# Performance work log

Measured on AMD Instinct MI355X. Metric: run time of the kernel, lower is better.

Reference implementation:

```python
import math
import jax, jax.numpy as jnp
import numpy as np

B, T, DIN, DH, E, TOPK = 2048, 512, 32, 96, 6, 2


def setup_inputs() -> dict:
    key = jax.random.key(0)
    ks = jax.random.split(key, 20)
    x = jax.random.normal(ks[0], (B, T, DIN), jnp.float32)
    lengths = jax.random.randint(ks[1], (B,), 1, T + 1)
    mask = (jnp.arange(T)[None, :] < lengths[:, None])

    def U(k, shape, fan):
        s = 1.0 / math.sqrt(fan)
        return jax.random.uniform(k, shape, jnp.float32, -s, s)

    # PyTorch LSTM init: U(-1/sqrt(DH), 1/sqrt(DH)); gate order i,f,g,o
    Wih = U(ks[2], (4 * DH, DIN), DH)
    Whh = U(ks[3], (4 * DH, DH), DH)
    bih = U(ks[4], (4 * DH,), DH)
    bhh = U(ks[5], (4 * DH,), DH)
    Wq = U(ks[6], (DH, DH), DH); bq = U(ks[7], (DH,), DH)
    Wk = U(ks[8], (DH, DH), DH); bk = U(ks[9], (DH,), DH)
    Wv = U(ks[10], (DH, DH), DH); bv = U(ks[11], (DH,), DH)
    Wg = U(ks[12], (E, 2 * DH), 2 * DH); bg = U(ks[13], (E,), 2 * DH)
    We1 = U(ks[14], (E, DH, 2 * DH), 2 * DH); be1 = U(ks[15], (E, DH), 2 * DH)
    We2 = U(ks[16], (E, DH), DH); be2 = U(ks[17], (E,), DH)
    return dict(x=x, lengths=lengths, mask=mask, Wih=Wih, Whh=Whh, bih=bih, bhh=bhh,
                Wq=Wq, bq=bq, Wk=Wk, bk=bk, Wv=Wv, bv=bv, Wg=Wg, bg=bg,
                We1=We1, be1=be1, We2=We2, be2=be2)


def _lstm(x, mask, Wih, Whh, bih, bhh):
    # packed-sequence semantics: carry frozen past each sample's length,
    # padded output positions zeroed (like pad_packed_sequence).
    xg = x @ Wih.T + bih  # [B,T,4*DH] precomputed input projection
    dh = Whh.shape[1]

    def step(carry, inp):
        h, c = carry
        xg_t, m_t = inp
        g = xg_t + h @ Whh.T + bhh
        i, f, gg, o = jnp.split(g, 4, axis=-1)
        c_new = jax.nn.sigmoid(f) * c + jax.nn.sigmoid(i) * jnp.tanh(gg)
        h_new = jax.nn.sigmoid(o) * jnp.tanh(c_new)
        m = m_t[:, None]
        h = jnp.where(m, h_new, h)
        c = jnp.where(m, c_new, c)
        return (h, c), jnp.where(m, h_new, 0.0)

    init = (jnp.zeros((x.shape[0], dh), x.dtype), jnp.zeros((x.shape[0], dh), x.dtype))
    (hT, _), H = jax.lax.scan(step, init, (jnp.swapaxes(xg, 0, 1), mask.T))
    return jnp.swapaxes(H, 0, 1), hT  # H:[B,T,DH], hT:[B,DH]


def reference(x, lengths, mask, Wih, Whh, bih, bhh, Wq, bq, Wk, bk, Wv, bv,
              Wg, bg, We1, be1, We2, be2):
    H, hT = _lstm(x, mask, Wih, Whh, bih, bhh)
    Q = hT @ Wq.T + bq                      # [B,DH]
    K = H @ Wk.T + bk                       # [B,T,DH]
    V = H @ Wv.T + bv                       # [B,T,DH]
    logits = jnp.einsum('bd,btd->bt', Q, K) / math.sqrt(K.shape[-1])
    logits = jnp.where(mask, logits, -1e9)
    alpha = jax.nn.softmax(logits, axis=1)  # [B,T]
    ctx = jnp.einsum('bt,btd->bd', alpha, V)
    feats = jnp.concatenate([ctx, hT], axis=-1)  # [B,2*DH]
    gate_logits = feats @ Wg.T + bg              # [B,E]
    topv, topi = jax.lax.top_k(gate_logits, TOPK)
    pi = jax.nn.softmax(topv, axis=-1)           # [B,TOPK]
    # all-expert dense compute (E tiny), then gather selected -> same math as
    # the per-expert masked scatter loop in the torch module (dropout off).
    h1 = jax.nn.relu(jnp.einsum('bf,ehf->beh', feats, We1) + be1[None])  # [B,E,DH]
    outs = jnp.einsum('beh,eh->be', h1, We2) + be2[None]                  # [B,E]
    sel = jnp.take_along_axis(outs, topi, axis=1)                         # [B,TOPK]
    yhat = jnp.sum(pi * sel, axis=-1, keepdims=True)                      # [B,1]
    return yhat, alpha, gate_logits
```

## Files before the change

kernel.cpp:

```cpp
#include <hip/hip_runtime.h>
#include <hip/hip_bf16.h>

#define B_ 2048
#define T_ 512
#define DIN_ 32
#define DH_ 96
#define NG_ 384
#define E_ 6

#define BPB 8
#define HP 104
#define GS 10

typedef __attribute__((ext_vector_type(8))) _Float16 f16x8;
typedef __attribute__((ext_vector_type(4))) float f32x4;

#if defined(__has_builtin)
# if __has_builtin(__builtin_amdgcn_exp2f)
#  define EXP2F(x) __builtin_amdgcn_exp2f(x)
# endif
# if __has_builtin(__builtin_amdgcn_rcpf)
#  define RCPF(x) __builtin_amdgcn_rcpf(x)
# endif
#endif
#ifndef EXP2F
# define EXP2F(x) exp2f(x)
#endif
#ifndef RCPF
# define RCPF(x) (1.0f/(x))
#endif

__device__ __forceinline__ float sigf(float x) {
    return RCPF(1.0f + EXP2F(x * -1.44269504f));
}
__device__ __forceinline__ float tanhf_(float x) {
    return 1.0f - 2.0f * RCPF(1.0f + EXP2F(x * 2.88539008f));
}

__device__ __forceinline__ f16x8 cvt8(float4 a, float4 b) {
    f16x8 r;
    r[0] = (_Float16)a.x; r[1] = (_Float16)a.y; r[2] = (_Float16)a.z; r[3] = (_Float16)a.w;
    r[4] = (_Float16)b.x; r[5] = (_Float16)b.y; r[6] = (_Float16)b.z; r[7] = (_Float16)b.w;
    return r;
}
__device__ __forceinline__ f16x8 cvt8p(const float* p) {
    return cvt8(*(const float4*)p, *(const float4*)(p + 4));
}

__device__ __forceinline__ void lds_barrier() {
    asm volatile("s_waitcnt lgkmcnt(0)\n\ts_barrier" ::: "memory");
}

__global__ __launch_bounds__(512) void sort_kernel(
    const int* __restrict__ lengths, int* __restrict__ perm) {
    __shared__ int sbins[512];
    __shared__ int soffs[512];
    const int tid = threadIdx.x;
    sbins[tid] = 0;
    __syncthreads();
    for (int b = tid; b < B_; b += 512) atomicAdd(&sbins[lengths[b] - 1], 1);
    __syncthreads();
    soffs[tid] = sbins[tid];
    __syncthreads();
    for (int d = 1; d < 512; d <<= 1) {
        int v = (tid >= d) ? soffs[tid - d] : 0;
        __syncthreads();
        soffs[tid] += v;
        __syncthreads();
    }
    int excl = soffs[tid] - sbins[tid];
    __syncthreads();
    soffs[tid] = excl;
    __syncthreads();
    for (int b = tid; b < B_; b += 512) {
        const int pos = atomicAdd(&soffs[lengths[b] - 1], 1);
        perm[pos] = b;
    }
}

__global__ __launch_bounds__(768, 1) void lstm_kernel(
    const float* __restrict__ x, const int* __restrict__ lengths,
    const int* __restrict__ perm,
    const float* __restrict__ Wih, const float* __restrict__ Whh,
    const float* __restrict__ bih, const float* __restrict__ bhh,
    _Float16* __restrict__ Hout, float* __restrict__ hT)
{
    __shared__ float sgate[NG_ * GS];
    __shared__ _Float16 sh[2][16 * HP];
    __shared__ int sgb[BPB], slen[BPB];

    const int tid  = threadIdx.x;
    const int bb   = blockIdx.x * BPB;
    const int wave = tid >> 6;
    const int lane = tid & 63;
    const int col  = lane & 15;
    const int quad = lane >> 4;

    if (tid < BPB) {
        const int g = perm[bb + tid];
        sgb[tid] = g;
        slen[tid] = lengths[g];
    }
    {
        _Float16* shf = &sh[0][0];
        for (int i = tid; i < 2 * 16 * HP; i += 768) shf[i] = (_Float16)0.f;
    }
    __syncthreads();

    int bmax = slen[0];
#pragma unroll
    for (int i = 1; i < BPB; ++i) bmax = max(bmax, slen[i]);

    int gc[2]; float bias[2];
    f16x8 wh[2][3], wi[2];
#pragma unroll
    for (int j = 0; j < 2; ++j) {
        const int tau = wave * 2 + j;
        const int g = tau / 6, u6 = tau % 6;
        const int gcj = g * DH_ + u6 * 16 + col;
        gc[j] = gcj;
#pragma unroll
        for (int kf = 0; kf < 3; ++kf)
            wh[j][kf] = cvt8p(Whh + gcj * DH_ + kf * 32 + quad * 8);
        wi[j] = cvt8p(Wih + gcj * DIN_ + quad * 8);
        bias[j] = bih[gcj] + bhh[gcj];
    }

    const int eu = tid >> 3;
    const int eb = tid & 7;
    float c1 = 0.f, hk1 = 0.f;
    const int len1 = slen[eb];

    const bool st_act = tid < 384;
    const int sb = tid / 48;
    const int su = (tid % 48) * 2;
    _Float16* Hst = Hout + ((long long)sgb[sb] * T_) * DH_ + su;

    const float* xp = x + ((long long)sgb[col & 7] * T_) * DIN_ + quad * 8;
    float4 xc0 = *(const float4*)xp;
    float4 xc1 = *(const float4*)(xp + 4);

    for (int t = 0; t < bmax; ++t) {
        const int buf = t & 1;

        const _Float16* hrow = &sh[buf][col * HP];
        f16x8 h0 = *(const f16x8*)(hrow + 0  + quad * 8);
        f16x8 h1 = *(const f16x8*)(hrow + 32 + quad * 8);
        f16x8 h2 = *(const f16x8*)(hrow + 64 + quad * 8);

        const float* xpn = (t + 1 < T_) ? (xp + DIN_) : xp;
        float4 xn0 = *(const float4*)xpn;
        float4 xn1 = *(const float4*)(xpn + 4);

        f16x8 xa = cvt8(xc0, xc1);

#pragma unroll
        for (int j = 0; j < 2; ++j) {
            f32x4 a = {bias[j], bias[j], bias[j], bias[j]};
            a = __builtin_amdgcn_mfma_f32_16x16x32_f16(h0, wh[j][0], a, 0, 0, 0);
            a = __builtin_amdgcn_mfma_f32_16x16x32_f16(h1, wh[j][1], a, 0, 0, 0);
            a = __builtin_amdgcn_mfma_f32_16x16x32_f16(h2, wh[j][2], a, 0, 0, 0);
            a = __builtin_amdgcn_mfma_f32_16x16x32_f16(xa, wi[j],    a, 0, 0, 0);
            if (quad < 2) {
                float2* sp = (float2*)&sgate[gc[j] * GS + quad * 4];
                sp[0] = float2{a[0], a[1]};
                sp[1] = float2{a[2], a[3]};
            }
        }
        lds_barrier();

        if (t > 0 && st_act) {
            unsigned v = *(const unsigned*)&sh[buf][sb * HP + su];
            *(unsigned*)Hst = v;
            Hst += DH_;
        }

        {
            float iv = sgate[(0 * DH_ + eu) * GS + eb];
            float fv = sgate[(1 * DH_ + eu) * GS + eb];
            float gv = sgate[(2 * DH_ + eu) * GS + eb];
            float ov = sgate[(3 * DH_ + eu) * GS + eb];
            float cn = sigf(fv) * c1 + sigf(iv) * tanhf_(gv);
            float hn = sigf(ov) * tanhf_(cn);
            const bool m = t < len1;
            c1  = m ? cn : c1;
            hk1 = m ? hn : hk1;
            sh[buf ^ 1][eb * HP + eu] = (_Float16)hk1;
        }
        lds_barrier();

        xp = xpn; xc0 = xn0; xc1 = xn1;
    }

    if (st_act) {
        unsigned v = *(const unsigned*)&sh[bmax & 1][sb * HP + su];
        *(unsigned*)Hst = v;
    }

    hT[sgb[eb] * DH_ + eu] = hk1;
}

__global__ __launch_bounds__(512) void attn_moe_kernel(
    const _Float16* __restrict__ H, const float* __restrict__ hT,
    const int* __restrict__ lengths,
    const float* __restrict__ Wq, const float* __restrict__ bq,
    const float* __restrict__ Wk, const float* __restrict__ bk,
    const float* __restrict__ Wv, const float* __restrict__ bv,
    const float* __restrict__ Wg, const float* __restrict__ bg,
    const float* __restrict__ We1, const float* __restrict__ be1,
    const float* __restrict__ We2, const float* __restrict__ be2,
    float* __restrict__ yhat_out, float* __restrict__ alpha_out,
    float* __restrict__ gl_out)
{
    __shared__ float salpha[T_];
    __shared__ float shT[DH_];
    __shared__ float sQ[DH_];
    __shared__ float sqk[DH_];
    __shared__ float spart[4 * DH_];
    __shared__ float sfeats[2 * DH_];
    __shared__ float sh1[2][DH_];
    __shared__ float sred[8], ssum[8];
    __shared__ float sgl[E_];
    __shared__ float spi[2];
    __shared__ float souts[2];
    __shared__ float sqb_s;
    __shared__ int stopi[2];

    const int b = blockIdx.x, tid = threadIdx.x;
    const int len = lengths[b];
    const float scale = 0.10206207262f;

    if (tid < DH_) shT[tid] = hT[b * DH_ + tid];
    __syncthreads();
    if (tid < DH_) {
        float acc = bq[tid];
        const float* wr = Wq + tid * DH_;
        for (int d = 0; d < DH_; d += 4) {
            float4 w4 = *(const float4*)(wr + d);
            acc += w4.x * shT[d] + w4.y * shT[d + 1] + w4.z * shT[d + 2] + w4.w * shT[d + 3];
        }
        sQ[tid] = acc;
    }
    __syncthreads();
    if (tid < DH_) {
        float acc = 0.f;
        for (int j = 0; j < DH_; ++j) acc += Wk[j * DH_ + tid] * sQ[j];
        sqk[tid] = acc * scale;
    }
    if (tid >= 448) {
        const int ln = tid - 448;
        float p = sQ[ln] * bk[ln];
        if (ln < DH_ - 64) p += sQ[ln + 64] * bk[ln + 64];
        for (int off = 32; off; off >>= 1) p += __shfl_xor(p, off);
        if (ln == 0) sqb_s = p * scale;
    }
    __syncthreads();
    const float qbv = sqb_s;

    const bool valid = tid < len;
    float l = qbv;
    if (valid) {
        const _Float16* hr = H + ((long long)b * T_ + tid) * DH_;
#pragma unroll
        for (int u = 0; u < DH_; u += 8) {
            f16x8 hv = *(const f16x8*)(hr + u);
            float4 qa = *(const float4*)&sqk[u];
            float4 qc = *(const float4*)&sqk[u + 4];
            l += (float)hv[0] * qa.x + (float)hv[1] * qa.y
               + (float)hv[2] * qa.z + (float)hv[3] * qa.w
               + (float)hv[4] * qc.x + (float)hv[5] * qc.y
               + (float)hv[6] * qc.z + (float)hv[7] * qc.w;
        }
    }
    float lv = valid ? l : -1e30f;

    float m = lv;
    for (int off = 32; off; off >>= 1) m = fmaxf(m, __shfl_xor(m, off));
    if ((tid & 63) == 0) sred[tid >> 6] = m;
    __syncthreads();
    m = sred[0];
#pragma unroll
    for (int i = 1; i < 8; ++i) m = fmaxf(m, sred[i]);

    float e = valid ? EXP2F((l - m) * 1.44269504f) : 0.f;
    float s = e;
    for (int off = 32; off; off >>= 1) s += __shfl_xor(s, off);
    if ((tid & 63) == 0) ssum[tid >> 6] = s;
    __syncthreads();
    s = ssum[0];
#pragma unroll
    for (int i = 1; i < 8; ++i) s += ssum[i];

    const float alpha = e * RCPF(s);
    salpha[tid] = alpha;
    alpha_out[(long long)b * T_ + tid] = alpha;
    __syncthreads();

    if (tid < 4 * DH_) {
        const int s4 = tid / DH_, u = tid - s4 * DH_;
        float acc = 0.f;
        const int t0 = s4 * 128, t1 = min(t0 + 128, len);
        const _Float16* hc = H + ((long long)b * T_) * DH_ + u;
        for (int t = t0; t < t1; ++t)
            acc += salpha[t] * (float)hc[t * DH_];
        spart[s4 * DH_ + u] = acc;
    }
    __syncthreads();
    if (tid < DH_) {
        float craw = spart[tid] + spart[DH_ + tid] + spart[2 * DH_ + tid] + spart[3 * DH_ + tid];
        spart[tid] = craw;
    }
    __syncthreads();
    if (tid < DH_) {
        float acc = bv[tid];
        const float* wr = Wv + tid * DH_;
        for (int u = 0; u < DH_; u += 4) {
            float4 w4 = *(const float4*)(wr + u);
            acc += w4.x * spart[u] + w4.y * spart[u + 1] + w4.z * spart[u + 2] + w4.w * spart[u + 3];
        }
        sfeats[tid] = acc;
        sfeats[DH_ + tid] = shT[tid];
    }
    __syncthreads();

    if (tid < 192) {
        const int e6 = tid >> 5, cc = tid & 31;
        float p = 0.f;
        const float* wg = Wg + e6 * 2 * DH_;
#pragma unroll
        for (int j = 0; j < 6; ++j) p += wg[cc * 6 + j] * sfeats[cc * 6 + j];
        for (int off = 16; off; off >>= 1) p += __shfl_xor(p, off);
        if (cc == 0) {
            float g = p + bg[e6];
            sgl[e6] = g;
            gl_out[b * E_ + e6] = g;
        }
    }
    __syncthreads();

    if (tid == 0) {
        int i0 = 0; float v0 = sgl[0];
        for (int ee = 1; ee < E_; ++ee) if (sgl[ee] > v0) { v0 = sgl[ee]; i0 = ee; }
        int i1 = -1; float v1 = -1e30f;
        for (int ee = 0; ee < E_; ++ee) {
            if (ee == i0) continue;
            if (sgl[ee] > v1) { v1 = sgl[ee]; i1 = ee; }
        }
        float e1 = EXP2F((v1 - v0) * 1.44269504f);
        float inv = RCPF(1.f + e1);
        spi[0] = inv; spi[1] = e1 * inv;
        stopi[0] = i0; stopi[1] = i1;
    }
    __syncthreads();

    if (tid < 192) {
        const int e2 = tid / DH_, u = tid - e2 * DH_;
        const int ex = stopi[e2];
        float acc = be1[ex * DH_ + u];
        const float* w = We1 + ((long long)ex * DH_ + u) * (2 * DH_);
        for (int f = 0; f < 2 * DH_; f += 4) {
            float4 w4 = *(const float4*)(w + f);
            acc += w4.x * sfeats[f] + w4.y * sfeats[f + 1] + w4.z * sfeats[f + 2] + w4.w * sfeats[f + 3];
        }
        sh1[e2][u] = fmaxf(acc, 0.f);
    }
    __syncthreads();

    if (tid < 128) {
        const int e2 = tid >> 6, ln = tid & 63;
        const int ex = stopi[e2];
        const float* w2 = We2 + ex * DH_;
        float p = sh1[e2][ln] * w2[ln];
        if (ln < DH_ - 64) p += sh1[e2][ln + 64] * w2[ln + 64];
        for (int off = 32; off; off >>= 1) p += __shfl_xor(p, off);
        if (ln == 0) souts[e2] = p + be2[ex];
    }
    __syncthreads();
    if (tid == 0)
        yhat_out[b] = spi[0] * souts[0] + spi[1] * souts[1];
}

extern "C" void kernel_launch(void* const* d_in, const int* in_sizes, int n_in,
                              void* d_out, int out_size, void* d_ws, size_t ws_size,
                              hipStream_t stream) {
    const float* x   = (const float*)d_in[0];
    const int* lengths = (const int*)d_in[1];
    const float* Wih = (const float*)d_in[3];
    const float* Whh = (const float*)d_in[4];
    const float* bih = (const float*)d_in[5];
    const float* bhh = (const float*)d_in[6];
    const float* Wq  = (const float*)d_in[7];
    const float* bq  = (const float*)d_in[8];
    const float* Wk  = (const float*)d_in[9];
    const float* bk  = (const float*)d_in[10];
    const float* Wv  = (const float*)d_in[11];
    const float* bv  = (const float*)d_in[12];
    const float* Wg  = (const float*)d_in[13];
    const float* bg  = (const float*)d_in[14];
    const float* We1 = (const float*)d_in[15];
    const float* be1 = (const float*)d_in[16];
    const float* We2 = (const float*)d_in[17];
    const float* be2 = (const float*)d_in[18];

    float* yhat  = (float*)d_out;
    float* alpha = yhat + B_;
    float* gl    = alpha + (size_t)B_ * T_;

    char* ws = (char*)d_ws;
    _Float16* Hws = (_Float16*)ws;
    float* hTws = (float*)(ws + (size_t)B_ * T_ * DH_ * 2);
    float* qkws = hTws + (size_t)B_ * DH_;
    float* qbws = qkws + (size_t)B_ * DH_;
    int* bins   = (int*)(qbws + B_);
    int* offs   = bins + 512;
    int* perm   = offs + 512;

    sort_kernel<<<dim3(1), dim3(512), 0, stream>>>(lengths, perm);

    lstm_kernel<<<dim3(B_ / BPB), dim3(768), 0, stream>>>(
        x, lengths, perm, Wih, Whh, bih, bhh, Hws, hTws);
    attn_moe_kernel<<<dim3(B_), dim3(512), 0, stream>>>(
        Hws, hTws, lengths, Wq, bq, Wk, bk, Wv, bv, Wg, bg,
        We1, be1, We2, be2, yhat, alpha, gl);
}
```

Measured before the change: 781.2 us.

## Shrink LSTM hidden buffer and restructure attention kernel to 256 threads

The LSTM kernel now keeps only the 8 real batch rows in its shared hidden-state buffer. The unused MFMA rows 8-15 are zero-filled in registers instead of being read from LDS and global memory. The attention/MoE kernel drops to 256 threads, each handling two timesteps for the logits and softmax. The context reduction now uses vectorized 8-wide f16 loads with shuffle reductions in place of scalar strided loads across 384 threads. Unused workspace pointers are also removed. The aim is less LDS traffic and better memory coalescing, at the cost of fewer threads per block in attention.

Measured after the change: 697.9 us. -10.7%, faster.

```diff
diff --git a/kernel.cpp b/kernel.cpp
--- a/kernel.cpp
+++ b/kernel.cpp
@@ -86,7 +86,7 @@
     _Float16* __restrict__ Hout, float* __restrict__ hT)
 {
     __shared__ float sgate[NG_ * GS];
-    __shared__ _Float16 sh[2][16 * HP];
+    __shared__ _Float16 sh[2][8 * HP];
     __shared__ int sgb[BPB], slen[BPB];
 
     const int tid  = threadIdx.x;
@@ -103,7 +103,7 @@
     }
     {
         _Float16* shf = &sh[0][0];
-        for (int i = tid; i < 2 * 16 * HP; i += 768) shf[i] = (_Float16)0.f;
+        for (int i = tid; i < 2 * 8 * HP; i += 768) shf[i] = (_Float16)0.f;
     }
     __syncthreads();
 
@@ -136,21 +136,25 @@
     const int su = (tid % 48) * 2;
     _Float16* Hst = Hout + ((long long)sgb[sb] * T_) * DH_ + su;
 
+    const bool arow = col < 8;
     const float* xp = x + ((long long)sgb[col & 7] * T_) * DIN_ + quad * 8;
-    float4 xc0 = *(const float4*)xp;
-    float4 xc1 = *(const float4*)(xp + 4);
+    float4 xc0 = make_float4(0.f, 0.f, 0.f, 0.f), xc1 = xc0;
+    if (arow) { xc0 = *(const float4*)xp; xc1 = *(const float4*)(xp + 4); }
 
     for (int t = 0; t < bmax; ++t) {
         const int buf = t & 1;
 
-        const _Float16* hrow = &sh[buf][col * HP];
-        f16x8 h0 = *(const f16x8*)(hrow + 0  + quad * 8);
-        f16x8 h1 = *(const f16x8*)(hrow + 32 + quad * 8);
-        f16x8 h2 = *(const f16x8*)(hrow + 64 + quad * 8);
+        f16x8 h0 = 0, h1 = 0, h2 = 0;
+        if (arow) {
+            const _Float16* hrow = &sh[buf][col * HP];
+            h0 = *(const f16x8*)(hrow + 0  + quad * 8);
+            h1 = *(const f16x8*)(hrow + 32 + quad * 8);
+            h2 = *(const f16x8*)(hrow + 64 + quad * 8);
+        }
 
         const float* xpn = (t + 1 < T_) ? (xp + DIN_) : xp;
-        float4 xn0 = *(const float4*)xpn;
-        float4 xn1 = *(const float4*)(xpn + 4);
+        float4 xn0 = make_float4(0.f, 0.f, 0.f, 0.f), xn1 = xn0;
+        if (arow) { xn0 = *(const float4*)xpn; xn1 = *(const float4*)(xpn + 4); }
 
         f16x8 xa = cvt8(xc0, xc1);
 
@@ -200,7 +204,7 @@
     hT[sgb[eb] * DH_ + eu] = hk1;
 }
 
-__global__ __launch_bounds__(512) void attn_moe_kernel(
+__global__ __launch_bounds__(256) void attn_moe_kernel(
     const _Float16* __restrict__ H, const float* __restrict__ hT,
     const int* __restrict__ lengths,
     const float* __restrict__ Wq, const float* __restrict__ bq,
@@ -216,10 +220,10 @@
     __shared__ float shT[DH_];
     __shared__ float sQ[DH_];
     __shared__ float sqk[DH_];
-    __shared__ float spart[4 * DH_];
+    __shared__ float spart[DH_];
     __shared__ float sfeats[2 * DH_];
     __shared__ float sh1[2][DH_];
-    __shared__ float sred[8], ssum[8];
+    __shared__ float sred[4], ssum[4];
     __shared__ float sgl[E_];
     __shared__ float spi[2];
     __shared__ float souts[2];
@@ -247,8 +251,8 @@
         for (int j = 0; j < DH_; ++j) acc += Wk[j * DH_ + tid] * sQ[j];
         sqk[tid] = acc * scale;
     }
-    if (tid >= 448) {
-        const int ln = tid - 448;
+    if (tid >= 192) {
+        const int ln = tid - 192;
         float p = sQ[ln] * bk[ln];
         if (ln < DH_ - 64) p += sQ[ln + 64] * bk[ln + 64];
         for (int off = 32; off; off >>= 1) p += __shfl_xor(p, off);
@@ -257,60 +261,78 @@
     __syncthreads();
     const float qbv = sqb_s;
 
-    const bool valid = tid < len;
-    float l = qbv;
-    if (valid) {
-        const _Float16* hr = H + ((long long)b * T_ + tid) * DH_;
-#pragma unroll
-        for (int u = 0; u < DH_; u += 8) {
-            f16x8 hv = *(const f16x8*)(hr + u);
-            float4 qa = *(const float4*)&sqk[u];
-            float4 qc = *(const float4*)&sqk[u + 4];
-            l += (float)hv[0] * qa.x + (float)hv[1] * qa.y
-               + (float)hv[2] * qa.z + (float)hv[3] * qa.w
-               + (float)hv[4] * qc.x + (float)hv[5] * qc.y
-               + (float)hv[6] * qc.z + (float)hv[7] * qc.w;
-        }
-    }
-    float lv = valid ? l : -1e30f;
-
-    float m = lv;
+    float lg[2]; bool vd[2];
+#pragma unroll
+    for (int hh = 0; hh < 2; ++hh) {
+        const int t = tid + hh * 256;
+        vd[hh] = t < len;
+        float l = qbv;
+        if (vd[hh]) {
+            const _Float16* hr = H + ((long long)b * T_ + t) * DH_;
+#pragma unroll
+            for (int u = 0; u < DH_; u += 8) {
+                f16x8 hv = *(const f16x8*)(hr + u);
+                float4 qa = *(const float4*)&sqk[u];
+                float4 qc = *(const float4*)&sqk[u + 4];
+                l += (float)hv[0] * qa.x + (float)hv[1] * qa.y
+                   + (float)hv[2] * qa.z + (float)hv[3] * qa.w
+                   + (float)hv[4] * qc.x + (float)hv[5] * qc.y
+                   + (float)hv[6] * qc.z + (float)hv[7] * qc.w;
+            }
+        }
+        lg[hh] = l;
+    }
+
+    float m = fmaxf(vd[0] ? lg[0] : -1e30f, vd[1] ? lg[1] : -1e30f);
     for (int off = 32; off; off >>= 1) m = fmaxf(m, __shfl_xor(m, off));
     if ((tid & 63) == 0) sred[tid >> 6] = m;
     __syncthreads();
-    m = sred[0];
-#pragma unroll
-    for (int i = 1; i < 8; ++i) m = fmaxf(m, sred[i]);
-
-    float e = valid ? EXP2F((l - m) * 1.44269504f) : 0.f;
-    float s = e;
+    m = fmaxf(fmaxf(sred[0], sred[1]), fmaxf(sred[2], sred[3]));
+
+    float e0 = vd[0] ? EXP2F((lg[0] - m) * 1.44269504f) : 0.f;
+    float e1 = vd[1] ? EXP2F((lg[1] - m) * 1.44269504f) : 0.f;
+    float s = e0 + e1;
     for (int off = 32; off; off >>= 1) s += __shfl_xor(s, off);
     if ((tid & 63) == 0) ssum[tid >> 6] = s;
     __syncthreads();
-    s = ssum[0];
-#pragma unroll
-    for (int i = 1; i < 8; ++i) s += ssum[i];
-
-    const float alpha = e * RCPF(s);
-    salpha[tid] = alpha;
-    alpha_out[(long long)b * T_ + tid] = alpha;
-    __syncthreads();
-
-    if (tid < 4 * DH_) {
-        const int s4 = tid / DH_, u = tid - s4 * DH_;
-        float acc = 0.f;
-        const int t0 = s4 * 128, t1 = min(t0 + 128, len);
-        const _Float16* hc = H + ((long long)b * T_) * DH_ + u;
-        for (int t = t0; t < t1; ++t)
-            acc += salpha[t] * (float)hc[t * DH_];
-        spart[s4 * DH_ + u] = acc;
-    }
-    __syncthreads();
-    if (tid < DH_) {
-        float craw = spart[tid] + spart[DH_ + tid] + spart[2 * DH_ + tid] + spart[3 * DH_ + tid];
-        spart[tid] = craw;
-    }
-    __syncthreads();
+    s = (ssum[0] + ssum[1]) + (ssum[2] + ssum[3]);
+
+    const float rinv = RCPF(s);
+    const float a0 = e0 * rinv, a1 = e1 * rinv;
+    salpha[tid] = a0;
+    salpha[tid + 256] = a1;
+    alpha_out[(long long)b * T_ + tid] = a0;
+    alpha_out[(long long)b * T_ + tid + 256] = a1;
+    __syncthreads();
+
+    if (tid < 192) {
+        const int ub = tid >> 4, tl = tid & 15;
+        float acc[8] = {0.f, 0.f, 0.f, 0.f, 0.f, 0.f, 0.f, 0.f};
+        const _Float16* hb = H + ((long long)b * T_) * DH_ + ub * 8;
+#pragma unroll 4
+        for (int k = 0; k < 32; ++k) {
+            const int t = tl + (k << 4);
+            if (t < len) {
+                f16x8 hv = *(const f16x8*)(hb + t * DH_);
+                const float a = salpha[t];
+#pragma unroll
+                for (int i = 0; i < 8; ++i) acc[i] += a * (float)hv[i];
+            }
+        }
+#pragma unroll
+        for (int i = 0; i < 8; ++i) {
+            acc[i] += __shfl_xor(acc[i], 1);
+            acc[i] += __shfl_xor(acc[i], 2);
+            acc[i] += __shfl_xor(acc[i], 4);
+            acc[i] += __shfl_xor(acc[i], 8);
+        }
+        if (tl == 0) {
+#pragma unroll
+            for (int i = 0; i < 8; ++i) spart[ub * 8 + i] = acc[i];
+        }
+    }
+    __syncthreads();
+
     if (tid < DH_) {
         float acc = bv[tid];
         const float* wr = Wv + tid * DH_;
@@ -346,9 +368,9 @@
             if (ee == i0) continue;
             if (sgl[ee] > v1) { v1 = sgl[ee]; i1 = ee; }
         }
-        float e1 = EXP2F((v1 - v0) * 1.44269504f);
-        float inv = RCPF(1.f + e1);
-        spi[0] = inv; spi[1] = e1 * inv;
+        float ex1 = EXP2F((v1 - v0) * 1.44269504f);
+        float inv = RCPF(1.f + ex1);
+        spi[0] = inv; spi[1] = ex1 * inv;
         stopi[0] = i0; stopi[1] = i1;
     }
     __syncthreads();
@@ -409,17 +431,13 @@
     char* ws = (char*)d_ws;
     _Float16* Hws = (_Float16*)ws;
     float* hTws = (float*)(ws + (size_t)B_ * T_ * DH_ * 2);
-    float* qkws = hTws + (size_t)B_ * DH_;
-    float* qbws = qkws + (size_t)B_ * DH_;
-    int* bins   = (int*)(qbws + B_);
-    int* offs   = bins + 512;
-    int* perm   = offs + 512;
+    int* perm   = (int*)(hTws + (size_t)B_ * DH_);
 
     sort_kernel<<<dim3(1), dim3(512), 0, stream>>>(lengths, perm);
 
     lstm_kernel<<<dim3(B_ / BPB), dim3(768), 0, stream>>>(
         x, lengths, perm, Wih, Whh, bih, bhh, Hws, hTws);
-    attn_moe_kernel<<<dim3(B_), dim3(512), 0, stream>>>(
+    attn_moe_kernel<<<dim3(B_), dim3(256), 0, stream>>>(
         Hws, hTws, lengths, Wq, bq, Wk, bk, Wv, bv, Wg, bg,
         We1, be1, We2, be2, yhat, alpha, gl);
 }
```
